# Kernel tuning notes

Measured on AMD Instinct MI355X. Metric: run time of the kernel, lower is better.

## Reference

```python
import jax, jax.numpy as jnp
import numpy as np

B, S, D, H = 4, 1024, 1024, 16
DH = D // H  # per-head dim


def setup_inputs() -> dict:
    key = jax.random.key(0)
    ks = jax.random.split(key, 9)
    f = lambda k, sh: jax.random.normal(k, sh, dtype=jnp.float32)
    return {
        "query": f(ks[0], (B, S, D)),
        "key": f(ks[1], (B, S, D)),
        "value": f(ks[2], (B, S, D)),
        "mask": jax.random.randint(ks[3], (B, S), 0, 2).astype(jnp.int32),
        "pos_emb": f(ks[4], (H, S, DH)),
        "W_q": f(ks[5], (D, D)) * 0.02,
        "W_k": f(ks[6], (D, D)) * 0.02,
        "W_v": f(ks[7], (D, D)) * 0.02,
        "W_o": f(ks[8], (D, D)) * 0.02,
    }


def _shift(x):
    """Music-Transformer skew trick. x: [b,h,i,j] -> [b,h,i,j]."""
    b, h, i, j = x.shape
    x = jnp.concatenate([x, jnp.zeros((b, h, i, i), x.dtype)], axis=-1)  # [b,h,i,i+j]
    l = i + j - 1
    flat = x.reshape(b, h, i * (i + j))
    pad = (-flat.shape[-1]) % l
    flat = jnp.concatenate([flat, jnp.zeros((b, h, pad), flat.dtype)], axis=-1)
    return flat.reshape(b, h, -1, l)[:, :, :i, i - 1:]


def reference(query, key, value, mask, pos_emb, W_q, W_k, W_v, W_o):
    b, s, _ = query.shape
    # torch Linear(bias=False): y = x @ W.T ; then split heads -> [b,h,s,dh]
    proj = lambda x, W: (x @ W.T).reshape(b, s, H, DH).transpose(0, 2, 1, 3)
    q = proj(query, W_q)
    k = proj(key, W_k)
    v = proj(value, W_v)

    dots = jnp.einsum('bhid,bhjd->bhij', q, k) * (DH ** -0.5)
    pe = pos_emb[:, :s, :]  # [h,s,dh]
    # NOTE: original code scales positional scores by dim ** (+0.5)
    pos_dots = jnp.einsum('bhid,hjd->bhij', q, pe) * (DH ** 0.5)
    dots = dots + _shift(pos_dots)

    m = (mask[:, :, None] * mask[:, None, :])[:, None]  # [b,1,s,s]
    dots = jnp.where(m == 0, jnp.float32(-1e9), dots)

    attn = jax.nn.softmax(dots, axis=-1)  # dropout omitted (eval / p=0)
    x = jnp.einsum('bhij,bhjd->bhid', attn, v)
    x = x.transpose(0, 2, 1, 3).reshape(b, s, H * DH)
    return x @ W_o.T
```

## Files before the change

### kernel.cpp

```cpp
#include <hip/hip_runtime.h>
#include <math.h>

#define BB 4
#define SS 1024
#define DD 1024
#define HH 16
#define DHH 64

typedef _Float16 half8 __attribute__((ext_vector_type(8)));
typedef _Float16 half4v __attribute__((ext_vector_type(4)));
typedef float v4f __attribute__((ext_vector_type(4)));
typedef unsigned int u32;
typedef unsigned short u16;

__device__ __forceinline__ void gload_lds16(const void* g, void* l) {
    __builtin_amdgcn_global_load_lds(
        (const __attribute__((address_space(1))) u32*)(const u32*)g,
        (__attribute__((address_space(3))) u32*)(u32*)l, 16, 0, 0);
}

__global__ __launch_bounds__(256) void convert_kernel(
    const float* __restrict__ wq, const float* __restrict__ wk,
    const float* __restrict__ wv, const float* __restrict__ wo,
    const float* __restrict__ pe, _Float16* __restrict__ dst)
{
    const int i4 = blockIdx.x * 256 + threadIdx.x;
    const int region = i4 >> 18;
    const int local4 = i4 & 262143;
    const float* srcs[5] = {wq, wk, wv, wo, pe};
    const float scales[5] = {1.0f, 0.125f, 1.0f, 1.0f, 8.0f};
    const float sc = scales[region];
    float4 v = *(const float4*)(srcs[region] + (size_t)local4 * 4);
    half4v h = {(_Float16)(v.x * sc), (_Float16)(v.y * sc),
                (_Float16)(v.z * sc), (_Float16)(v.w * sc)};
    *(half4v*)(dst + ((size_t)region << 20) + (size_t)local4 * 4) = h;
}

__global__ __launch_bounds__(256) void convert2_kernel(
    const float* __restrict__ wq, const float* __restrict__ wk,
    const float* __restrict__ wv, const float* __restrict__ wo,
    const float* __restrict__ pe, const float* __restrict__ q,
    const float* __restrict__ k, const float* __restrict__ vv,
    _Float16* __restrict__ dst)
{
    const int i4 = blockIdx.x * 256 + threadIdx.x;
    const int region = i4 >> 18;
    const int local4 = i4 & 262143;
    const float* src;
    float sc = 1.0f;
    if (region == 0)      { src = wq; }
    else if (region == 1) { src = wk; sc = 0.125f; }
    else if (region == 2) { src = wv; }
    else if (region == 3) { src = wo; }
    else if (region == 4) { src = pe; sc = 8.0f; }
    else if (region < 9)  { src = q  + ((size_t)(region - 5)  << 20); }
    else if (region < 13) { src = k  + ((size_t)(region - 9)  << 20); }
    else                  { src = vv + ((size_t)(region - 13) << 20); }
    float4 v = *(const float4*)(src + (size_t)local4 * 4);
    half4v h = {(_Float16)(v.x * sc), (_Float16)(v.y * sc),
                (_Float16)(v.z * sc), (_Float16)(v.w * sc)};
    *(half4v*)(dst + ((size_t)region << 20) + (size_t)local4 * 4) = h;
}

__global__ __launch_bounds__(256) void gemm_proj_f32(
    const float* __restrict__ Aq, const float* __restrict__ Ak,
    const float* __restrict__ Av,
    const _Float16* __restrict__ Wqf, const _Float16* __restrict__ Wkf,
    const _Float16* __restrict__ Wvf,
    _Float16* __restrict__ Cq, _Float16* __restrict__ Ck,
    _Float16* __restrict__ Cv)
{
    __shared__ _Float16 As[128 * 32];
    __shared__ _Float16 Bs[64 * 32];

    const int z = blockIdx.z;
    const float* A = z == 0 ? Aq : z == 1 ? Ak : Av;
    const _Float16* W = z == 0 ? Wqf : z == 1 ? Wkf : Wvf;
    _Float16* C = z == 0 ? Cq : z == 1 ? Ck : Cv;

    const int tid = threadIdx.x;
    const int w = tid >> 6, lane = tid & 63, lm = lane & 15, quad = lane >> 4;
    const int n0 = blockIdx.x * 64, m0 = blockIdx.y * 128;

    const int brow = tid >> 2, blc = (tid & 3) ^ (brow & 3);

    v4f zero4 = {0.f, 0.f, 0.f, 0.f};
    v4f acc[2][4];
#pragma unroll
    for (int mi = 0; mi < 2; mi++)
#pragma unroll
        for (int ni = 0; ni < 4; ni++) acc[mi][ni] = zero4;

    for (int k0 = 0; k0 < DD; k0 += 32) {
        __syncthreads();
        gload_lds16(W + (size_t)(n0 + brow) * DD + k0 + blc * 8, Bs + tid * 8);
#pragma unroll
        for (int u = 0; u < 4; u++) {
            int c4 = tid + 256 * u;
            int row = c4 >> 3, k4 = c4 & 7;
            float4 v = *(const float4*)(A + (size_t)(m0 + row) * DD + k0 + k4 * 4);
            half4v hv = {(_Float16)v.x, (_Float16)v.y, (_Float16)v.z, (_Float16)v.w};
            int c16 = k4 >> 1, hlf = k4 & 1;
            *(half4v*)(As + row * 32 + (((c16 ^ (row & 3)) << 3) + (hlf << 2))) = hv;
        }
        __syncthreads();

        half8 af[2], bf[4];
#pragma unroll
        for (int mi = 0; mi < 2; mi++) {
            int row = w * 32 + mi * 16 + lm;
            af[mi] = *(const half8*)(As + row * 32 + ((quad ^ (row & 3)) << 3));
        }
#pragma unroll
        for (int ni = 0; ni < 4; ni++) {
            int row = ni * 16 + lm;
            bf[ni] = *(const half8*)(Bs + row * 32 + ((quad ^ (row & 3)) << 3));
        }
#pragma unroll
        for (int mi = 0; mi < 2; mi++)
#pragma unroll
            for (int ni = 0; ni < 4; ni++)
                acc[mi][ni] = __builtin_amdgcn_mfma_f32_16x16x32_f16(
                    af[mi], bf[ni], acc[mi][ni], 0, 0, 0);
    }

    const int h = n0 >> 6;
#pragma unroll
    for (int mi = 0; mi < 2; mi++)
#pragma unroll
        for (int r = 0; r < 4; r++) {
            int m = m0 + w * 32 + mi * 16 + quad * 4 + r;
            int b = m >> 10, s = m & 1023;
            size_t base = ((size_t)(b * HH + h) * SS + s) * DHH;
#pragma unroll
            for (int ni = 0; ni < 4; ni++)
                C[base + ni * 16 + lm] = (_Float16)acc[mi][ni][r];
        }
}

__global__ __launch_bounds__(256) void gemm_proj_f16_128(
    const _Float16* __restrict__ Aq, const _Float16* __restrict__ Ak,
    const _Float16* __restrict__ Av,
    const _Float16* __restrict__ Wqf, const _Float16* __restrict__ Wkf,
    const _Float16* __restrict__ Wvf,
    _Float16* __restrict__ Cq, _Float16* __restrict__ Ck,
    _Float16* __restrict__ Cv)
{
    __shared__ _Float16 As[128 * 32];
    __shared__ _Float16 Bs[128 * 32];

    const int z = blockIdx.z;
    const _Float16* A = z == 0 ? Aq : z == 1 ? Ak : Av;
    const _Float16* W = z == 0 ? Wqf : z == 1 ? Wkf : Wvf;
    _Float16* C = z == 0 ? Cq : z == 1 ? Ck : Cv;

    const int tid = threadIdx.x;
    const int w = tid >> 6, lane = tid & 63, lm = lane & 15, quad = lane >> 4;
    const int wr = (w >> 1) * 64, wc = (w & 1) * 64;
    const int n0 = blockIdx.x * 128, m0 = blockIdx.y * 128;

    v4f zero4 = {0.f, 0.f, 0.f, 0.f};
    v4f acc[4][4];
#pragma unroll
    for (int mi = 0; mi < 4; mi++)
#pragma unroll
        for (int ni = 0; ni < 4; ni++) acc[mi][ni] = zero4;

    for (int k0 = 0; k0 < DD; k0 += 32) {
        __syncthreads();
#pragma unroll
        for (int u = 0; u < 2; u++) {
            int p = tid + 256 * u;
            int row = p >> 2, lc = (p & 3) ^ (row & 3);
            gload_lds16(W + (size_t)(n0 + row) * DD + k0 + lc * 8, Bs + p * 8);
            gload_lds16(A + (size_t)(m0 + row) * DD + k0 + lc * 8, As + p * 8);
        }
        __syncthreads();

        half8 af[4], bf[4];
#pragma unroll
        for (int mi = 0; mi < 4; mi++) {
            int row = wr + mi * 16 + lm;
            af[mi] = *(const half8*)(As + row * 32 + ((quad ^ (row & 3)) << 3));
        }
#pragma unroll
        for (int ni = 0; ni < 4; ni++) {
            int row = wc + ni * 16 + lm;
            bf[ni] = *(const half8*)(Bs + row * 32 + ((quad ^ (row & 3)) << 3));
        }
#pragma unroll
        for (int mi = 0; mi < 4; mi++)
#pragma unroll
            for (int ni = 0; ni < 4; ni++)
                acc[mi][ni] = __builtin_amdgcn_mfma_f32_16x16x32_f16(
                    af[mi], bf[ni], acc[mi][ni], 0, 0, 0);
    }

#pragma unroll
    for (int mi = 0; mi < 4; mi++)
#pragma unroll
        for (int r = 0; r < 4; r++) {
            int m = m0 + wr + mi * 16 + quad * 4 + r;
            int b = m >> 10, s = m & 1023;
#pragma unroll
            for (int ni = 0; ni < 4; ni++) {
                int n = n0 + wc + ni * 16 + lm;
                int h = n >> 6, d = n & 63;
                C[((size_t)(b * HH + h) * SS + s) * DHH + d] = (_Float16)acc[mi][ni][r];
            }
        }
}

__global__ __launch_bounds__(256) void gemm_out_128(
    const _Float16* __restrict__ A, const _Float16* __restrict__ W,
    float* __restrict__ C)
{
    __shared__ _Float16 As[128 * 32];
    __shared__ _Float16 Bs[128 * 32];

    const int tid = threadIdx.x;
    const int w = tid >> 6, lane = tid & 63, lm = lane & 15, quad = lane >> 4;
    const int wr = (w >> 1) * 64, wc = (w & 1) * 64;
    const int n0 = blockIdx.x * 128, m0 = blockIdx.y * 128;

    v4f zero4 = {0.f, 0.f, 0.f, 0.f};
    v4f acc[4][4];
#pragma unroll
    for (int mi = 0; mi < 4; mi++)
#pragma unroll
        for (int ni = 0; ni < 4; ni++) acc[mi][ni] = zero4;

    for (int k0 = 0; k0 < DD; k0 += 32) {
        __syncthreads();
#pragma unroll
        for (int u = 0; u < 2; u++) {
            int p = tid + 256 * u;
            int row = p >> 2, lc = (p & 3) ^ (row & 3);
            gload_lds16(W + (size_t)(n0 + row) * DD + k0 + lc * 8, Bs + p * 8);
            gload_lds16(A + (size_t)(m0 + row) * DD + k0 + lc * 8, As + p * 8);
        }
        __syncthreads();

        half8 af[4], bf[4];
#pragma unroll
        for (int mi = 0; mi < 4; mi++) {
            int row = wr + mi * 16 + lm;
            af[mi] = *(const half8*)(As + row * 32 + ((quad ^ (row & 3)) << 3));
        }
#pragma unroll
        for (int ni = 0; ni < 4; ni++) {
            int row = wc + ni * 16 + lm;
            bf[ni] = *(const half8*)(Bs + row * 32 + ((quad ^ (row & 3)) << 3));
        }
#pragma unroll
        for (int mi = 0; mi < 4; mi++)
#pragma unroll
            for (int ni = 0; ni < 4; ni++)
                acc[mi][ni] = __builtin_amdgcn_mfma_f32_16x16x32_f16(
                    af[mi], bf[ni], acc[mi][ni], 0, 0, 0);
    }

#pragma unroll
    for (int mi = 0; mi < 4; mi++)
#pragma unroll
        for (int r = 0; r < 4; r++) {
            size_t base = (size_t)(m0 + wr + mi * 16 + quad * 4 + r) * DD
                        + n0 + wc + lm;
#pragma unroll
            for (int ni = 0; ni < 4; ni++)
                C[base + ni * 16] = acc[mi][ni][r];
        }
}

__global__ __launch_bounds__(256) void gemm_out(
    const _Float16* __restrict__ A, const _Float16* __restrict__ W,
    float* __restrict__ C)
{
    __shared__ _Float16 As[128 * 32];
    __shared__ _Float16 Bs[64 * 32];

    const int tid = threadIdx.x;
    const int w = tid >> 6, lane = tid & 63, lm = lane & 15, quad = lane >> 4;
    const int n0 = blockIdx.x * 64, m0 = blockIdx.y * 128;
    const int brow = tid >> 2, blc = (tid & 3) ^ (brow & 3);

    v4f zero4 = {0.f, 0.f, 0.f, 0.f};
    v4f acc[2][4];
#pragma unroll
    for (int mi = 0; mi < 2; mi++)
#pragma unroll
        for (int ni = 0; ni < 4; ni++) acc[mi][ni] = zero4;

    for (int k0 = 0; k0 < DD; k0 += 32) {
        __syncthreads();
        gload_lds16(W + (size_t)(n0 + brow) * DD + k0 + blc * 8, Bs + tid * 8);
#pragma unroll
        for (int u = 0; u < 2; u++) {
            int p = tid + 256 * u;
            int row = p >> 2, lc = (p & 3) ^ (row & 3);
            gload_lds16(A + (size_t)(m0 + row) * DD + k0 + lc * 8, As + p * 8);
        }
        __syncthreads();

        half8 af[2], bf[4];
#pragma unroll
    for (int mi = 0; mi < 2; mi++) {
            int row = w * 32 + mi * 16 + lm;
            af[mi] = *(const half8*)(As + row * 32 + ((quad ^ (row & 3)) << 3));
        }
#pragma unroll
        for (int ni = 0; ni < 4; ni++) {
            int row = ni * 16 + lm;
            bf[ni] = *(const half8*)(Bs + row * 32 + ((quad ^ (row & 3)) << 3));
        }
#pragma unroll
        for (int mi = 0; mi < 2; mi++)
#pragma unroll
            for (int ni = 0; ni < 4; ni++)
                acc[mi][ni] = __builtin_amdgcn_mfma_f32_16x16x32_f16(
                    af[mi], bf[ni], acc[mi][ni], 0, 0, 0);
    }

#pragma unroll
    for (int mi = 0; mi < 2; mi++)
#pragma unroll
        for (int r = 0; r < 4; r++) {
            size_t base = (size_t)(m0 + w * 32 + mi * 16 + quad * 4 + r) * DD
                        + n0 + lm;
#pragma unroll
            for (int ni = 0; ni < 4; ni++)
                C[base + ni * 16] = acc[mi][ni][r];
        }
}

__global__ __launch_bounds__(256) void attn_mfma(
    const _Float16* __restrict__ Qg, const _Float16* __restrict__ Kg,
    const _Float16* __restrict__ Vg, const int* __restrict__ mask,
    const _Float16* __restrict__ peg, _Float16* __restrict__ Og)
{
    __shared__ _Float16 Ks[64 * 64];
    __shared__ _Float16 Vt[64 * 64];
    __shared__ _Float16 PEb[128 * 64];
    __shared__ _Float16 Pb[4][16 * 64];

    const int tid = threadIdx.x;
    const int w = tid >> 6, lane = tid & 63;
    const int lm = lane & 15, quad = lane >> 4;

    const int lid = blockIdx.y * 16 + blockIdx.x;
    const int it = ((lid & 15) + ((lid >> 8) << 2)) & 15;
    const int bh = lid >> 4;
    const int i0 = it * 64;
    const int b = bh >> 4, h = bh & 15;

    const _Float16* Qb = Qg + (size_t)bh * SS * DHH;
    const _Float16* Kb = Kg + (size_t)bh * SS * DHH;
    const _Float16* Vb = Vg + (size_t)bh * SS * DHH;
    const _Float16* peh = peg + (size_t)h * SS * DHH;

    float mi_f[4];
#pragma unroll
    for (int r = 0; r < 4; r++)
        mi_f[r] = (float)mask[b * SS + i0 + w * 16 + quad * 4 + r];

    half8 qf[2];
#pragma unroll
    for (int kc = 0; kc < 2; kc++)
        qf[kc] = *(const half8*)(Qb + (size_t)(i0 + w * 16 + lm) * DHH
                                 + kc * 32 + quad * 8);

    const int srow = tid >> 3, sk8 = tid & 7;
    const int lmx = (lm & 7) << 3;

    half8 ones8 = {(_Float16)1, (_Float16)1, (_Float16)1, (_Float16)1,
                   (_Float16)1, (_Float16)1, (_Float16)1, (_Float16)1};

    v4f zero4 = {0.f, 0.f, 0.f, 0.f};
    float m_run[4];
    v4f oacc[4], lacc;
#pragma unroll
    for (int r = 0; r < 4; r++) m_run[r] = -1e30f;
#pragma unroll
    for (int nb = 0; nb < 4; nb++) oacc[nb] = zero4;
    lacc = zero4;

    half8 kreg[2], vreg[2], pereg[4];
#pragma unroll
    for (int u = 0; u < 2; u++) {
        int row = srow + 32 * u;
        kreg[u] = *(const half8*)(Kb + (size_t)row * DHH + sk8 * 8);
        vreg[u] = *(const half8*)(Vb + (size_t)row * DHH + sk8 * 8);
    }
    {
        const int g0 = SS - 1 - i0 - 63;
#pragma unroll
        for (int u = 0; u < 4; u++) {
            int o = srow + 32 * u;
            int g = g0 + o;
            half8 v = {0, 0, 0, 0, 0, 0, 0, 0};
            if (g < SS) v = *(const half8*)(peh + (size_t)g * DHH + sk8 * 8);
            pereg[u] = v;
        }
    }

    for (int jt = 0; jt < SS / 64; jt++) {
        const int j0 = jt * 64;
        const bool do_pe = (jt <= it);
        __syncthreads();

#pragma unroll
        for (int u = 0; u < 2; u++) {
            int row = srow + 32 * u;
            *(half8*)(Ks + row * 64 + ((sk8 * 8) ^ ((row & 7) << 3))) = kreg[u];
        }
#pragma unroll
        for (int u = 0; u < 2; u++) {
            int row = srow + 32 * u;
            int jsw = row ^ (sk8 << 3);
#pragma unroll
            for (int e = 0; e < 8; e++) Vt[(sk8 * 8 + e) * 64 + jsw] = vreg[u][e];
        }
        if (do_pe) {
#pragma unroll
            for (int u = 0; u < 4; u++) {
                int o = srow + 32 * u;
                *(half8*)(PEb + o * 64 + ((sk8 * 8) ^ ((o & 7) << 3))) = pereg[u];
            }
        }
        float mj_f[4];
#pragma unroll
        for (int nb = 0; nb < 4; nb++)
            mj_f[nb] = (float)mask[b * SS + j0 + nb * 16 + lm];
        __syncthreads();

        if (jt + 1 < SS / 64) {
            const int j0n = j0 + 64;
#pragma unroll
            for (int u = 0; u < 2; u++) {
                int row = srow + 32 * u;
                kreg[u] = *(const half8*)(Kb + (size_t)(j0n + row) * DHH + sk8 * 8);
                vreg[u] = *(const half8*)(Vb + (size_t)(j0n + row) * DHH + sk8 * 8);
            }
            if (jt + 1 <= it) {
                const int g0n = SS - 1 + j0n - i0 - 63;
#pragma unroll
                for (int u = 0; u < 4; u++) {
                    int o = srow + 32 * u;
                    int g = g0n + o;
                    half8 v = {0, 0, 0, 0, 0, 0, 0, 0};
                    if (g < SS) v = *(const half8*)(peh + (size_t)g * DHH + sk8 * 8);
                    pereg[u] = v;
                }
            }
        }

        v4f sacc[4];
#pragma unroll
        for (int nb = 0; nb < 4; nb++) sacc[nb] = zero4;
        __builtin_amdgcn_s_setprio(1);
#pragma unroll
        for (int nb = 0; nb < 4; nb++)
#pragma unroll
            for (int kc = 0; kc < 2; kc++) {
                half8 kf = *(const half8*)(Ks + (nb * 16 + lm) * 64
                                           + ((kc * 32 + quad * 8) ^ lmx));
                sacc[nb] = __builtin_amdgcn_mfma_f32_16x16x32_f16(qf[kc], kf, sacc[nb], 0, 0, 0);
            }
        __builtin_amdgcn_s_setprio(0);

        if (do_pe) {
            v4f racc[5];
#pragma unroll
            for (int e = 0; e < 5; e++) racc[e] = zero4;
            __builtin_amdgcn_s_setprio(1);
#pragma unroll
            for (int e = 0; e < 5; e++) {
                int row = (e + 3 - w) * 16 + lm;
#pragma unroll
                for (int kc = 0; kc < 2; kc++) {
                    half8 pf = *(const half8*)(PEb + row * 64
                                               + ((kc * 32 + quad * 8) ^ lmx));
                    racc[e] = __builtin_amdgcn_mfma_f32_16x16x32_f16(qf[kc], pf, racc[e], 0, 0, 0);
                }
            }
            __builtin_amdgcn_s_setprio(0);
#pragma unroll
            for (int nb = 0; nb < 4; nb++)
#pragma unroll
                for (int r = 0; r < 4; r++) {
                    int qr = quad * 4 + r;
                    float vsrc = (((lm + qr + 1) & 15) <= qr)
                               ? racc[nb][r] : racc[nb + 1][r];
                    int src = (lane & 48) | ((lm - qr - 1) & 15);
                    sacc[nb][r] += __shfl(vsrc, src);
                }
        }

        float p[4][4];
        float alpha[4];
#pragma unroll
        for (int i = 0; i < 4; i++) {
            float mi = mi_f[i];
            float rmax = -1e30f;
#pragma unroll
            for (int j = 0; j < 4; j++) {
                float s = sacc[j][i];
                if (mi * mj_f[j] == 0.f) s = -1e9f;
                sacc[j][i] = s;
                rmax = fmaxf(rmax, s);
            }
#pragma unroll
            for (int off = 1; off < 16; off <<= 1)
                rmax = fmaxf(rmax, __shfl_xor(rmax, off));
            float mnew = fmaxf(m_run[i], rmax);
            alpha[i] = __expf(m_run[i] - mnew);
            m_run[i] = mnew;
#pragma unroll
            for (int j = 0; j < 4; j++)
                p[j][i] = __expf(sacc[j][i] - mnew);
        }

        _Float16* Pw = &Pb[w][0];
#pragma unroll
        for (int nb = 0; nb < 4; nb++)
#pragma unroll
            for (int r = 0; r < 4; r++) {
                int qr = quad * 4 + r;
                Pw[qr * 64 + ((nb * 16 + lm) ^ ((qr & 7) << 3))] = (_Float16)p[nb][r];
            }
#pragma unroll
        for (int nb = 0; nb < 4; nb++)
#pragma unroll
            for (int r = 0; r < 4; r++) oacc[nb][r] *= alpha[r];
#pragma unroll
        for (int r = 0; r < 4; r++) lacc[r] *= alpha[r];

        __builtin_amdgcn_s_setprio(1);
#pragma unroll
        for (int kc = 0; kc < 2; kc++) {
            half8 pfrag = *(const half8*)(Pw + lm * 64 + ((kc * 32 + quad * 8) ^ lmx));
            lacc = __builtin_amdgcn_mfma_f32_16x16x32_f16(pfrag, ones8, lacc, 0, 0, 0);
#pragma unroll
            for (int nb = 0; nb < 4; nb++) {
                int d = nb * 16 + lm;
                int col = (kc * 32 + quad * 8) ^ (((d >> 3) & 7) << 3);
                half8 vfrag = *(const half8*)(Vt + d * 64 + col);
                oacc[nb] = __builtin_amdgcn_mfma_f32_16x16x32_f16(pfrag, vfrag, oacc[nb], 0, 0, 0);
            }
        }
        __builtin_amdgcn_s_setprio(0);
    }

#pragma unroll
    for (int r = 0; r < 4; r++) {
        float inv = 1.f / lacc[r];
        int s = i0 + w * 16 + quad * 4 + r;
#pragma unroll
        for (int nb = 0; nb < 4; nb++)
            Og[((size_t)b * SS + s) * DD + h * DHH + nb * 16 + lm] =
                (_Float16)(oacc[nb][r] * inv);
    }
}

extern "C" void kernel_launch(void* const* d_in, const int* in_sizes, int n_in,
                              void* d_out, int out_size, void* d_ws, size_t ws_size,
                              hipStream_t stream)
{
    const float* query = (const float*)d_in[0];
    const float* key   = (const float*)d_in[1];
    const float* value = (const float*)d_in[2];
    const int*   mask  = (const int*)d_in[3];
    const float* pe    = (const float*)d_in[4];
    const float* Wq    = (const float*)d_in[5];
    const float* Wk    = (const float*)d_in[6];
    const float* Wv    = (const float*)d_in[7];
    const float* Wo    = (const float*)d_in[8];
    float* out = (float*)d_out;

    _Float16* ws16 = (_Float16*)d_ws;
    const size_t MEG = 1048576;
    _Float16* wqf = ws16;
    _Float16* wkf = ws16 + 1 * MEG;
    _Float16* wvf = ws16 + 2 * MEG;
    _Float16* wof = ws16 + 3 * MEG;
    _Float16* pef = ws16 + 4 * MEG;

    const bool big = ws_size >= (size_t)33 * MEG * sizeof(_Float16);

    if (big) {
        _Float16* q16 = ws16 + 5 * MEG;
        _Float16* k16 = ws16 + 9 * MEG;
        _Float16* v16 = ws16 + 13 * MEG;
        _Float16* qp  = ws16 + 17 * MEG;
        _Float16* kp  = ws16 + 21 * MEG;
        _Float16* vp  = ws16 + 25 * MEG;
        _Float16* ao  = ws16 + 29 * MEG;

        convert2_kernel<<<17408, 256, 0, stream>>>(
            Wq, Wk, Wv, Wo, pe, query, key, value, ws16);

        gemm_proj_f16_128<<<dim3(DD / 128, (BB * SS) / 128, 3), 256, 0, stream>>>(
            q16, k16, v16, wqf, wkf, wvf, qp, kp, vp);

        attn_mfma<<<dim3(SS / 64, BB * HH), 256, 0, stream>>>(
            qp, kp, vp, mask, pef, ao);

        gemm_out_128<<<dim3(DD / 128, (BB * SS) / 128), 256, 0, stream>>>(ao, wof, out);
    } else {
        _Float16* qp  = ws16 + 5 * MEG;
        _Float16* kp  = ws16 + 9 * MEG;
        _Float16* vp  = ws16 + 13 * MEG;
        _Float16* ao  = ws16 + 17 * MEG;

        convert_kernel<<<5120, 256, 0, stream>>>(Wq, Wk, Wv, Wo, pe, ws16);

        gemm_proj_f32<<<dim3(DD / 64, (BB * SS) / 128, 3), 256, 0, stream>>>(
            query, key, value, wqf, wkf, wvf, qp, kp, vp);

        attn_mfma<<<dim3(SS / 64, BB * HH), 256, 0, stream>>>(
            qp, kp, vp, mask, pef, ao);

        gemm_out<<<dim3(DD / 64, (BB * SS) / 128), 256, 0, stream>>>(ao, wof, out);
    }
}
```

Baseline: 272.7 us.

## Read K and PE fragments directly from global memory, double-buffer V in LDS

The attention kernel stops staging K and positional-embedding tiles through shared memory and loads the MFMA fragments straight from global memory (L2/L1-cached). PE is re-laid out per head with 64 zero-padded rows so the out-of-range branch disappears. V keeps an LDS transpose, now double-buffered, which drops the leading barrier, and launch bounds request 4 blocks per CU. The gain is less LDS traffic, fewer barriers and higher occupancy, at the cost of uncoalesced, latency-exposed global fragment loads and a workspace layout change (ao now aliases q16).

```diff
diff --git a/kernel.cpp b/kernel.cpp
--- a/kernel.cpp
+++ b/kernel.cpp
@@ -6,6 +6,7 @@
 #define DD 1024
 #define HH 16
 #define DHH 64
+#define PEROWS 1088
 
 typedef _Float16 half8 __attribute__((ext_vector_type(8)));
 typedef _Float16 half4v __attribute__((ext_vector_type(4)));
@@ -24,16 +25,31 @@
     const float* __restrict__ wv, const float* __restrict__ wo,
     const float* __restrict__ pe, _Float16* __restrict__ dst)
 {
-    const int i4 = blockIdx.x * 256 + threadIdx.x;
+    const int blk = blockIdx.x;
+    if (blk >= 5120) {
+        int j = (blk - 5120) * 256 + threadIdx.x;
+        int p = j * 4;
+        int h = p >> 12, wd = p & 4095;
+        half4v z = {(_Float16)0, (_Float16)0, (_Float16)0, (_Float16)0};
+        *(half4v*)(dst + (size_t)4194304 + (size_t)h * (PEROWS * 64) + 65536 + wd) = z;
+        return;
+    }
+    const int i4 = blk * 256 + threadIdx.x;
     const int region = i4 >> 18;
     const int local4 = i4 & 262143;
     const float* srcs[5] = {wq, wk, wv, wo, pe};
     const float scales[5] = {1.0f, 0.125f, 1.0f, 1.0f, 8.0f};
     const float sc = scales[region];
     float4 v = *(const float4*)(srcs[region] + (size_t)local4 * 4);
-    half4v h = {(_Float16)(v.x * sc), (_Float16)(v.y * sc),
-                (_Float16)(v.z * sc), (_Float16)(v.w * sc)};
-    *(half4v*)(dst + ((size_t)region << 20) + (size_t)local4 * 4) = h;
+    half4v h4 = {(_Float16)(v.x * sc), (_Float16)(v.y * sc),
+                 (_Float16)(v.z * sc), (_Float16)(v.w * sc)};
+    if (region == 4) {
+        int idx = local4 * 4;
+        int h = idx >> 16, row = (idx >> 6) & 1023, col = idx & 63;
+        *(half4v*)(dst + (size_t)4194304 + (size_t)h * (PEROWS * 64) + row * 64 + col) = h4;
+    } else {
+        *(half4v*)(dst + ((size_t)region << 20) + (size_t)local4 * 4) = h4;
+    }
 }
 
 __global__ __launch_bounds__(256) void convert2_kernel(
@@ -43,7 +59,16 @@
     const float* __restrict__ k, const float* __restrict__ vv,
     _Float16* __restrict__ dst)
 {
-    const int i4 = blockIdx.x * 256 + threadIdx.x;
+    const int blk = blockIdx.x;
+    if (blk >= 17408) {
+        int j = (blk - 17408) * 256 + threadIdx.x;
+        int p = j * 4;
+        int h = p >> 12, wd = p & 4095;
+        half4v z = {(_Float16)0, (_Float16)0, (_Float16)0, (_Float16)0};
+        *(half4v*)(dst + (size_t)4194304 + (size_t)h * (PEROWS * 64) + 65536 + wd) = z;
+        return;
+    }
+    const int i4 = blk * 256 + threadIdx.x;
     const int region = i4 >> 18;
     const int local4 = i4 & 262143;
     const float* src;
@@ -57,9 +82,17 @@
     else if (region < 13) { src = k  + ((size_t)(region - 9)  << 20); }
     else                  { src = vv + ((size_t)(region - 13) << 20); }
     float4 v = *(const float4*)(src + (size_t)local4 * 4);
-    half4v h = {(_Float16)(v.x * sc), (_Float16)(v.y * sc),
-                (_Float16)(v.z * sc), (_Float16)(v.w * sc)};
-    *(half4v*)(dst + ((size_t)region << 20) + (size_t)local4 * 4) = h;
+    half4v h4 = {(_Float16)(v.x * sc), (_Float16)(v.y * sc),
+                 (_Float16)(v.z * sc), (_Float16)(v.w * sc)};
+    if (region == 4) {
+        int idx = local4 * 4;
+        int h = idx >> 16, row = (idx >> 6) & 1023, col = idx & 63;
+        *(half4v*)(dst + (size_t)4194304 + (size_t)h * (PEROWS * 64) + row * 64 + col) = h4;
+    } else if (region >= 5) {
+        *(half4v*)(dst + ((size_t)region << 20) + 65536 + (size_t)local4 * 4) = h4;
+    } else {
+        *(half4v*)(dst + ((size_t)region << 20) + (size_t)local4 * 4) = h4;
+    }
 }
 
 __global__ __launch_bounds__(256) void gemm_proj_f32(
@@ -333,14 +366,13 @@
         }
 }
 
-__global__ __launch_bounds__(256) void attn_mfma(
+__global__ __launch_bounds__(256, 4) void attn_mfma(
     const _Float16* __restrict__ Qg, const _Float16* __restrict__ Kg,
     const _Float16* __restrict__ Vg, const int* __restrict__ mask,
-    const _Float16* __restrict__ peg, _Float16* __restrict__ Og)
-{
-    __shared__ _Float16 Ks[64 * 64];
-    __shared__ _Float16 Vt[64 * 64];
-    __shared__ _Float16 PEb[128 * 64];
+    const _Float16* __restrict__ peg,
+    _Float16* __restrict__ Og)
+{
+    __shared__ _Float16 Vt[2][64 * 64];
     __shared__ _Float16 Pb[4][16 * 64];
 
     const int tid = threadIdx.x;
@@ -356,7 +388,7 @@
     const _Float16* Qb = Qg + (size_t)bh * SS * DHH;
     const _Float16* Kb = Kg + (size_t)bh * SS * DHH;
     const _Float16* Vb = Vg + (size_t)bh * SS * DHH;
-    const _Float16* peh = peg + (size_t)h * SS * DHH;
+    const _Float16* peh = peg + (size_t)h * PEROWS * DHH;
 
     float mi_f[4];
 #pragma unroll
@@ -384,48 +416,22 @@
     for (int nb = 0; nb < 4; nb++) oacc[nb] = zero4;
     lacc = zero4;
 
-    half8 kreg[2], vreg[2], pereg[4];
-#pragma unroll
-    for (int u = 0; u < 2; u++) {
-        int row = srow + 32 * u;
-        kreg[u] = *(const half8*)(Kb + (size_t)row * DHH + sk8 * 8);
-        vreg[u] = *(const half8*)(Vb + (size_t)row * DHH + sk8 * 8);
-    }
-    {
-        const int g0 = SS - 1 - i0 - 63;
-#pragma unroll
-        for (int u = 0; u < 4; u++) {
-            int o = srow + 32 * u;
-            int g = g0 + o;
-            half8 v = {0, 0, 0, 0, 0, 0, 0, 0};
-            if (g < SS) v = *(const half8*)(peh + (size_t)g * DHH + sk8 * 8);
-            pereg[u] = v;
-        }
-    }
+    half8 vreg[2];
+#pragma unroll
+    for (int u = 0; u < 2; u++)
+        vreg[u] = *(const half8*)(Vb + (size_t)(srow + 32 * u) * DHH + sk8 * 8);
 
     for (int jt = 0; jt < SS / 64; jt++) {
         const int j0 = jt * 64;
         const bool do_pe = (jt <= it);
-        __syncthreads();
-
-#pragma unroll
-        for (int u = 0; u < 2; u++) {
-            int row = srow + 32 * u;
-            *(half8*)(Ks + row * 64 + ((sk8 * 8) ^ ((row & 7) << 3))) = kreg[u];
-        }
+
+        _Float16* Vtb = &Vt[jt & 1][0];
 #pragma unroll
         for (int u = 0; u < 2; u++) {
             int row = srow + 32 * u;
             int jsw = row ^ (sk8 << 3);
 #pragma unroll
-            for (int e = 0; e < 8; e++) Vt[(sk8 * 8 + e) * 64 + jsw] = vreg[u][e];
-        }
-        if (do_pe) {
-#pragma unroll
-            for (int u = 0; u < 4; u++) {
-                int o = srow + 32 * u;
-                *(half8*)(PEb + o * 64 + ((sk8 * 8) ^ ((o & 7) << 3))) = pereg[u];
-            }
+            for (int e = 0; e < 8; e++) Vtb[(sk8 * 8 + e) * 64 + jsw] = vreg[u][e];
         }
         float mj_f[4];
 #pragma unroll
@@ -436,22 +442,8 @@
         if (jt + 1 < SS / 64) {
             const int j0n = j0 + 64;
 #pragma unroll
-            for (int u = 0; u < 2; u++) {
-                int row = srow + 32 * u;
-                kreg[u] = *(const half8*)(Kb + (size_t)(j0n + row) * DHH + sk8 * 8);
-                vreg[u] = *(const half8*)(Vb + (size_t)(j0n + row) * DHH + sk8 * 8);
-            }
-            if (jt + 1 <= it) {
-                const int g0n = SS - 1 + j0n - i0 - 63;
-#pragma unroll
-                for (int u = 0; u < 4; u++) {
-                    int o = srow + 32 * u;
-                    int g = g0n + o;
-                    half8 v = {0, 0, 0, 0, 0, 0, 0, 0};
-                    if (g < SS) v = *(const half8*)(peh + (size_t)g * DHH + sk8 * 8);
-                    pereg[u] = v;
-                }
-            }
+            for (int u = 0; u < 2; u++)
+                vreg[u] = *(const half8*)(Vb + (size_t)(j0n + srow + 32 * u) * DHH + sk8 * 8);
         }
 
         v4f sacc[4];
@@ -462,13 +454,14 @@
         for (int nb = 0; nb < 4; nb++)
 #pragma unroll
             for (int kc = 0; kc < 2; kc++) {
-                half8 kf = *(const half8*)(Ks + (nb * 16 + lm) * 64
-                                           + ((kc * 32 + quad * 8) ^ lmx));
+                half8 kf = *(const half8*)(Kb + (size_t)(j0 + nb * 16 + lm) * DHH
+                                           + kc * 32 + quad * 8);
                 sacc[nb] = __builtin_amdgcn_mfma_f32_16x16x32_f16(qf[kc], kf, sacc[nb], 0, 0, 0);
             }
         __builtin_amdgcn_s_setprio(0);
 
         if (do_pe) {
+            const int g0 = SS - 1 + j0 - i0 - 63;
             v4f racc[5];
 #pragma unroll
             for (int e = 0; e < 5; e++) racc[e] = zero4;
@@ -478,8 +471,8 @@
                 int row = (e + 3 - w) * 16 + lm;
 #pragma unroll
                 for (int kc = 0; kc < 2; kc++) {
-                    half8 pf = *(const half8*)(PEb + row * 64
-                                               + ((kc * 32 + quad * 8) ^ lmx));
+                    half8 pf = *(const half8*)(peh + (size_t)(g0 + row) * DHH
+                                               + kc * 32 + quad * 8);
                     racc[e] = __builtin_amdgcn_mfma_f32_16x16x32_f16(qf[kc], pf, racc[e], 0, 0, 0);
                 }
             }
@@ -544,7 +537,7 @@
             for (int nb = 0; nb < 4; nb++) {
                 int d = nb * 16 + lm;
                 int col = (kc * 32 + quad * 8) ^ (((d >> 3) & 7) << 3);
-                half8 vfrag = *(const half8*)(Vt + d * 64 + col);
+                half8 vfrag = *(const half8*)(Vtb + d * 64 + col);
                 oacc[nb] = __builtin_amdgcn_mfma_f32_16x16x32_f16(pfrag, vfrag, oacc[nb], 0, 0, 0);
             }
         }
@@ -583,42 +576,43 @@
     _Float16* wkf = ws16 + 1 * MEG;
     _Float16* wvf = ws16 + 2 * MEG;
     _Float16* wof = ws16 + 3 * MEG;
-    _Float16* pef = ws16 + 4 * MEG;
+    _Float16* pep = ws16 + 4 * MEG;
+    const size_t QB = 5 * MEG + 65536;
 
     const bool big = ws_size >= (size_t)33 * MEG * sizeof(_Float16);
 
     if (big) {
-        _Float16* q16 = ws16 + 5 * MEG;
-        _Float16* k16 = ws16 + 9 * MEG;
-        _Float16* v16 = ws16 + 13 * MEG;
-        _Float16* qp  = ws16 + 17 * MEG;
-        _Float16* kp  = ws16 + 21 * MEG;
-        _Float16* vp  = ws16 + 25 * MEG;
-        _Float16* ao  = ws16 + 29 * MEG;
-
-        convert2_kernel<<<17408, 256, 0, stream>>>(
+        _Float16* q16 = ws16 + QB;
+        _Float16* k16 = ws16 + QB + 4 * MEG;
+        _Float16* v16 = ws16 + QB + 8 * MEG;
+        _Float16* qp  = ws16 + QB + 12 * MEG;
+        _Float16* kp  = ws16 + QB + 16 * MEG;
+        _Float16* vp  = ws16 + QB + 20 * MEG;
+        _Float16* ao  = q16;
+
+        convert2_kernel<<<17472, 256, 0, stream>>>(
             Wq, Wk, Wv, Wo, pe, query, key, value, ws16);
 
         gemm_proj_f16_128<<<dim3(DD / 128, (BB * SS) / 128, 3), 256, 0, stream>>>(
             q16, k16, v16, wqf, wkf, wvf, qp, kp, vp);
 
         attn_mfma<<<dim3(SS / 64, BB * HH), 256, 0, stream>>>(
-            qp, kp, vp, mask, pef, ao);
+            qp, kp, vp, mask, pep, ao);
 
         gemm_out_128<<<dim3(DD / 128, (BB * SS) / 128), 256, 0, stream>>>(ao, wof, out);
     } else {
-        _Float16* qp  = ws16 + 5 * MEG;
-        _Float16* kp  = ws16 + 9 * MEG;
-        _Float16* vp  = ws16 + 13 * MEG;
-        _Float16* ao  = ws16 + 17 * MEG;
-
-        convert_kernel<<<5120, 256, 0, stream>>>(Wq, Wk, Wv, Wo, pe, ws16);
+        _Float16* qp  = ws16 + QB;
+        _Float16* kp  = ws16 + QB + 4 * MEG;
+        _Float16* vp  = ws16 + QB + 8 * MEG;
+        _Float16* ao  = ws16 + QB + 12 * MEG;
+
+        convert_kernel<<<5184, 256, 0, stream>>>(Wq, Wk, Wv, Wo, pe, ws16);
 
         gemm_proj_f32<<<dim3(DD / 64, (BB * SS) / 128, 3), 256, 0, stream>>>(
             query, key, value, wqf, wkf, wvf, qp, kp, vp);
 
         attn_mfma<<<dim3(SS / 64, BB * HH), 256, 0, stream>>>(
-            qp, kp, vp, mask, pef, ao);
+            qp, kp, vp, mask, pep, ao);
 
         gemm_out<<<dim3(DD / 64, (BB * SS) / 128), 256, 0, stream>>>(ao, wof, out);
     }
```

Measured after the change: 332.0 us. 1.22x slower.

## Widen attention key/value tile from 64 to 128 columns per iteration

Applied to the files above, without the earlier changes.

The flash-attention loop now processes 128 keys per iteration instead of 64. K, V, positional-embedding and P buffers in shared memory and registers are doubled or enlarged to match. The relative-position shift is done in two 64-column halves, and the P store is fused into the exp loop. This halves the number of loop iterations and barriers and gives the MFMAs more work per sync. In exchange, shared-memory use grows from about 40KB to 72KB and register pressure rises, which may lower occupancy.

```diff
diff --git a/kernel.cpp b/kernel.cpp
--- a/kernel.cpp
+++ b/kernel.cpp
@@ -338,10 +338,10 @@
     const _Float16* __restrict__ Vg, const int* __restrict__ mask,
     const _Float16* __restrict__ peg, _Float16* __restrict__ Og)
 {
-    __shared__ _Float16 Ks[64 * 64];
-    __shared__ _Float16 Vt[64 * 64];
-    __shared__ _Float16 PEb[128 * 64];
-    __shared__ _Float16 Pb[4][16 * 64];
+    __shared__ _Float16 Ks[128 * 64];
+    __shared__ _Float16 Vt[64 * 128];
+    __shared__ _Float16 PEb[192 * 64];
+    __shared__ _Float16 Pb[4][16 * 128];
 
     const int tid = threadIdx.x;
     const int w = tid >> 6, lane = tid & 63;
@@ -384,9 +384,9 @@
     for (int nb = 0; nb < 4; nb++) oacc[nb] = zero4;
     lacc = zero4;
 
-    half8 kreg[2], vreg[2], pereg[4];
-#pragma unroll
-    for (int u = 0; u < 2; u++) {
+    half8 kreg[4], vreg[4], pereg[6];
+#pragma unroll
+    for (int u = 0; u < 4; u++) {
         int row = srow + 32 * u;
         kreg[u] = *(const half8*)(Kb + (size_t)row * DHH + sk8 * 8);
         vreg[u] = *(const half8*)(Vb + (size_t)row * DHH + sk8 * 8);
@@ -394,57 +394,57 @@
     {
         const int g0 = SS - 1 - i0 - 63;
 #pragma unroll
-        for (int u = 0; u < 4; u++) {
+        for (int u = 0; u < 6; u++) {
             int o = srow + 32 * u;
             int g = g0 + o;
             half8 v = {0, 0, 0, 0, 0, 0, 0, 0};
-            if (g < SS) v = *(const half8*)(peh + (size_t)g * DHH + sk8 * 8);
+            if (g >= 0 && g < SS) v = *(const half8*)(peh + (size_t)g * DHH + sk8 * 8);
             pereg[u] = v;
         }
     }
 
-    for (int jt = 0; jt < SS / 64; jt++) {
-        const int j0 = jt * 64;
-        const bool do_pe = (jt <= it);
-        __syncthreads();
-
-#pragma unroll
-        for (int u = 0; u < 2; u++) {
+    for (int jt = 0; jt < SS / 128; jt++) {
+        const int j0 = jt * 128;
+        const bool do_pe = (2 * jt <= it);
+        __syncthreads();
+
+#pragma unroll
+        for (int u = 0; u < 4; u++) {
             int row = srow + 32 * u;
             *(half8*)(Ks + row * 64 + ((sk8 * 8) ^ ((row & 7) << 3))) = kreg[u];
         }
 #pragma unroll
-        for (int u = 0; u < 2; u++) {
+        for (int u = 0; u < 4; u++) {
             int row = srow + 32 * u;
             int jsw = row ^ (sk8 << 3);
 #pragma unroll
-            for (int e = 0; e < 8; e++) Vt[(sk8 * 8 + e) * 64 + jsw] = vreg[u][e];
+            for (int e = 0; e < 8; e++) Vt[(sk8 * 8 + e) * 128 + jsw] = vreg[u][e];
         }
         if (do_pe) {
 #pragma unroll
-            for (int u = 0; u < 4; u++) {
+            for (int u = 0; u < 6; u++) {
                 int o = srow + 32 * u;
                 *(half8*)(PEb + o * 64 + ((sk8 * 8) ^ ((o & 7) << 3))) = pereg[u];
             }
         }
-        float mj_f[4];
-#pragma unroll
-        for (int nb = 0; nb < 4; nb++)
+        float mj_f[8];
+#pragma unroll
+        for (int nb = 0; nb < 8; nb++)
             mj_f[nb] = (float)mask[b * SS + j0 + nb * 16 + lm];
         __syncthreads();
 
-        if (jt + 1 < SS / 64) {
-            const int j0n = j0 + 64;
-#pragma unroll
-            for (int u = 0; u < 2; u++) {
+        if (jt + 1 < SS / 128) {
+            const int j0n = j0 + 128;
+#pragma unroll
+            for (int u = 0; u < 4; u++) {
                 int row = srow + 32 * u;
                 kreg[u] = *(const half8*)(Kb + (size_t)(j0n + row) * DHH + sk8 * 8);
                 vreg[u] = *(const half8*)(Vb + (size_t)(j0n + row) * DHH + sk8 * 8);
             }
-            if (jt + 1 <= it) {
+            if (2 * (jt + 1) <= it) {
                 const int g0n = SS - 1 + j0n - i0 - 63;
 #pragma unroll
-                for (int u = 0; u < 4; u++) {
+                for (int u = 0; u < 6; u++) {
                     int o = srow + 32 * u;
                     int g = g0n + o;
                     half8 v = {0, 0, 0, 0, 0, 0, 0, 0};
@@ -454,12 +454,12 @@
             }
         }
 
-        v4f sacc[4];
-#pragma unroll
-        for (int nb = 0; nb < 4; nb++) sacc[nb] = zero4;
+        v4f sacc[8];
+#pragma unroll
+        for (int nb = 0; nb < 8; nb++) sacc[nb] = zero4;
         __builtin_amdgcn_s_setprio(1);
 #pragma unroll
-        for (int nb = 0; nb < 4; nb++)
+        for (int nb = 0; nb < 8; nb++)
 #pragma unroll
             for (int kc = 0; kc < 2; kc++) {
                 half8 kf = *(const half8*)(Ks + (nb * 16 + lm) * 64
@@ -494,16 +494,42 @@
                     int src = (lane & 48) | ((lm - qr - 1) & 15);
                     sacc[nb][r] += __shfl(vsrc, src);
                 }
-        }
-
-        float p[4][4];
+            v4f raccB[5];
+            raccB[0] = racc[4];
+#pragma unroll
+            for (int e = 1; e < 5; e++) raccB[e] = zero4;
+            __builtin_amdgcn_s_setprio(1);
+#pragma unroll
+            for (int e = 1; e < 5; e++) {
+                int row = (e + 7 - w) * 16 + lm;
+#pragma unroll
+                for (int kc = 0; kc < 2; kc++) {
+                    half8 pf = *(const half8*)(PEb + row * 64
+                                               + ((kc * 32 + quad * 8) ^ lmx));
+                    raccB[e] = __builtin_amdgcn_mfma_f32_16x16x32_f16(qf[kc], pf, raccB[e], 0, 0, 0);
+                }
+            }
+            __builtin_amdgcn_s_setprio(0);
+#pragma unroll
+            for (int nb = 4; nb < 8; nb++)
+#pragma unroll
+                for (int r = 0; r < 4; r++) {
+                    int qr = quad * 4 + r;
+                    float vsrc = (((lm + qr + 1) & 15) <= qr)
+                               ? raccB[nb - 4][r] : raccB[nb - 3][r];
+                    int src = (lane & 48) | ((lm - qr - 1) & 15);
+                    sacc[nb][r] += __shfl(vsrc, src);
+                }
+        }
+
         float alpha[4];
+        _Float16* Pw = &Pb[w][0];
 #pragma unroll
         for (int i = 0; i < 4; i++) {
             float mi = mi_f[i];
             float rmax = -1e30f;
 #pragma unroll
-            for (int j = 0; j < 4; j++) {
+            for (int j = 0; j < 8; j++) {
                 float s = sacc[j][i];
                 if (mi * mj_f[j] == 0.f) s = -1e9f;
                 sacc[j][i] = s;
@@ -515,36 +541,30 @@
             float mnew = fmaxf(m_run[i], rmax);
             alpha[i] = __expf(m_run[i] - mnew);
             m_run[i] = mnew;
-#pragma unroll
-            for (int j = 0; j < 4; j++)
-                p[j][i] = __expf(sacc[j][i] - mnew);
-        }
-
-        _Float16* Pw = &Pb[w][0];
+            int qr = quad * 4 + i;
+#pragma unroll
+            for (int j = 0; j < 8; j++) {
+                float pv = __expf(sacc[j][i] - mnew);
+                Pw[qr * 128 + ((j * 16 + lm) ^ ((qr & 7) << 3))] = (_Float16)pv;
+            }
+        }
 #pragma unroll
         for (int nb = 0; nb < 4; nb++)
 #pragma unroll
-            for (int r = 0; r < 4; r++) {
-                int qr = quad * 4 + r;
-                Pw[qr * 64 + ((nb * 16 + lm) ^ ((qr & 7) << 3))] = (_Float16)p[nb][r];
-            }
-#pragma unroll
-        for (int nb = 0; nb < 4; nb++)
-#pragma unroll
             for (int r = 0; r < 4; r++) oacc[nb][r] *= alpha[r];
 #pragma unroll
         for (int r = 0; r < 4; r++) lacc[r] *= alpha[r];
 
         __builtin_amdgcn_s_setprio(1);
 #pragma unroll
-        for (int kc = 0; kc < 2; kc++) {
-            half8 pfrag = *(const half8*)(Pw + lm * 64 + ((kc * 32 + quad * 8) ^ lmx));
+        for (int kc = 0; kc < 4; kc++) {
+            half8 pfrag = *(const half8*)(Pw + lm * 128 + ((kc * 32 + quad * 8) ^ lmx));
             lacc = __builtin_amdgcn_mfma_f32_16x16x32_f16(pfrag, ones8, lacc, 0, 0, 0);
 #pragma unroll
             for (int nb = 0; nb < 4; nb++) {
                 int d = nb * 16 + lm;
                 int col = (kc * 32 + quad * 8) ^ (((d >> 3) & 7) << 3);
-                half8 vfrag = *(const half8*)(Vt + d * 64 + col);
+                half8 vfrag = *(const half8*)(Vt + d * 128 + col);
                 oacc[nb] = __builtin_amdgcn_mfma_f32_16x16x32_f16(pfrag, vfrag, oacc[nb], 0, 0, 0);
             }
         }
```

After: 310.7 us. 1.14x slower.
